# Kernel tuning notes

Hardware: AMD Instinct MI355X
Metric: run time of the kernel (lower is better)

The kernel has to match this reference:

```python
import jax, jax.numpy as jnp
from jax import lax
import numpy as np

N, C, H, W = 8, 128, 96, 96
G, K = 8, 3                      # groups, kernel_size
GC = C // G                      # group channels = 16
STRIDE, PAD, DIL = 1, 1, 1
OFFSET_SCALE = 1.0
OM_DIM = int(np.ceil(G * K * K * 3 / 8) * 8)   # 216 (== G*K*K*3, no padding)
GN_EPS = 1e-5


def setup_inputs() -> dict:
    key = jax.random.key(0)
    ks = jax.random.split(key, 7)
    inp = {
        "input": jax.random.normal(ks[0], (N, C, H, W), dtype=jnp.float32),
        # depthwise conv (Conv2d groups=C): OIHW with I=1
        "dw_w": jax.random.normal(ks[1], (C, 1, K, K), dtype=jnp.float32) * 0.1,
        "dw_b": jax.random.normal(ks[2], (C,), dtype=jnp.float32) * 0.05,
        # GroupNorm(num_groups=1) affine params
        "gn_w": jnp.ones((C,), dtype=jnp.float32),
        "gn_b": jnp.zeros((C,), dtype=jnp.float32),
        # offset_mask Linear (module zero-inits; use small random for a meaningful test)
        "om_w": jax.random.normal(ks[3], (OM_DIM, C), dtype=jnp.float32) * 0.02,
        "om_b": jax.random.normal(ks[4], (OM_DIM,), dtype=jnp.float32) * 0.02,
    }
    return inp


def _dcnv4_forward(x, dw_w, dw_b, gn_w, gn_b, om_w, om_b):
    # x: (N, C, H, W)
    # ---- offset/mask branch: depthwise conv -> GroupNorm(1) -> GELU -> Linear
    x1 = lax.conv_general_dilated(
        x, dw_w, window_strides=(1, 1), padding=[(1, 1), (1, 1)],
        feature_group_count=C, dimension_numbers=("NCHW", "OIHW", "NCHW"))
    x1 = x1 + dw_b[None, :, None, None]
    mu = jnp.mean(x1, axis=(1, 2, 3), keepdims=True)
    var = jnp.var(x1, axis=(1, 2, 3), keepdims=True)
    x1 = (x1 - mu) * lax.rsqrt(var + GN_EPS)
    x1 = x1 * gn_w[None, :, None, None] + gn_b[None, :, None, None]
    x1 = jax.nn.gelu(x1, approximate=False)
    x1 = jnp.transpose(x1, (0, 2, 3, 1))                     # (N,H,W,C)
    om = jnp.einsum("nhwc,oc->nhwo", x1, om_w) + om_b        # (N,H,W,216)

    K2 = K * K
    om = om[..., : G * K2 * 3].reshape(N, H, W, G, K2 * 3)
    offs = om[..., : 2 * K2].reshape(N, H, W, G, K2, 2)      # (dx, dy) per point
    mask = om[..., 2 * K2:]                                  # (N,H,W,G,K2), no softmax in DCNv4

    # ---- sampling locations (pixel coords in the unpadded input, zeros outside)
    ky, kx = jnp.meshgrid(jnp.arange(K), jnp.arange(K), indexing="ij")
    base_y = ((ky - (K - 1) / 2.0) * DIL).reshape(-1).astype(jnp.float32)  # (K2,)
    base_x = ((kx - (K - 1) / 2.0) * DIL).reshape(-1).astype(jnp.float32)
    ctr_y = jnp.arange(H, dtype=jnp.float32) * STRIDE - PAD + DIL * (K - 1) / 2.0
    ctr_x = jnp.arange(W, dtype=jnp.float32) * STRIDE - PAD + DIL * (K - 1) / 2.0
    loc_y = ctr_y[None, :, None, None, None] + (base_y + offs[..., 1]) * OFFSET_SCALE
    loc_x = ctr_x[None, None, :, None, None] + (base_x + offs[..., 0]) * OFFSET_SCALE

    # ---- grouped bilinear gather
    xv = jnp.transpose(x, (0, 2, 3, 1)).reshape(N, H, W, G, GC)   # values, channels-last
    y0 = jnp.floor(loc_y)
    x0 = jnp.floor(loc_x)
    ly = loc_y - y0
    lx = loc_x - x0
    y0i = y0.astype(jnp.int32)
    x0i = x0.astype(jnp.int32)
    n_idx = jnp.arange(N)[:, None, None, None, None]
    g_idx = jnp.arange(G)[None, None, None, :, None]

    def gather(yi, xi):
        valid = (yi >= 0) & (yi < H) & (xi >= 0) & (xi < W)
        yc = jnp.clip(yi, 0, H - 1)
        xc = jnp.clip(xi, 0, W - 1)
        v = xv[n_idx, yc, xc, g_idx]                 # (N,H,W,G,K2,GC)
        return v * valid[..., None].astype(xv.dtype)

    samp = (gather(y0i,     x0i)     * ((1 - ly) * (1 - lx))[..., None]
          + gather(y0i,     x0i + 1) * ((1 - ly) * lx)[..., None]
          + gather(y0i + 1, x0i)     * (ly * (1 - lx))[..., None]
          + gather(y0i + 1, x0i + 1) * (ly * lx)[..., None])

    out = jnp.sum(samp * mask[..., None], axis=4)    # (N,H,W,G,GC)
    out = out.reshape(N, H, W, C)
    return jnp.transpose(out, (0, 3, 1, 2))          # (N,C,H,W)


def reference(input, dw_w, dw_b, gn_w, gn_b, om_w, om_b):
    return _dcnv4_forward(input, dw_w, dw_b, gn_w, gn_b, om_w, om_b)
```

## Files before the change

kernel.cpp:

```cpp
#include <hip/hip_runtime.h>

#define N_   8
#define C_   128
#define H_   96
#define W_   96
#define G_   8
#define GC_  16
#define HW_  (H_ * W_)
#define CHW_ (C_ * HW_)
#define OM_  216
#define OMP_ 224
#define OMROWS2_ 112
#define EPS_ 1e-5f
#define BLKS_PER_N_ 1152

typedef short bf16x8 __attribute__((ext_vector_type(8)));
typedef float f32x4 __attribute__((ext_vector_type(4)));

static __device__ __forceinline__ unsigned short f2bf(float f) {
  unsigned int u = __float_as_uint(f);
  unsigned int r = (u + 0x7fffu + ((u >> 16) & 1u)) >> 16;
  return (unsigned short)r;
}
static __device__ __forceinline__ float lo_bf(unsigned int u) {
  return __uint_as_float(u << 16);
}
static __device__ __forceinline__ float hi_bf(unsigned int u) {
  return __uint_as_float(u & 0xffff0000u);
}

__global__ __launch_bounds__(256) void k_front(const float* __restrict__ x,
                                               const float* __restrict__ dw_w,
                                               const float* __restrict__ dw_b,
                                               float* __restrict__ xg,
                                               unsigned short* __restrict__ x1b,
                                               float2* __restrict__ partials) {
  __shared__ float tile_c[32][33];
  __shared__ float tile_a[32][33];
  __shared__ float ls[4], lq[4];
  int tx = threadIdx.x;
  int ty = threadIdx.y;
  int p0 = blockIdx.x * 32;
  int c0 = blockIdx.y * 32;
  int n = blockIdx.z;
  int p = p0 + tx;
  int h = p / W_;
  int w = p - h * W_;

  float s = 0.0f, q = 0.0f;
#pragma unroll
  for (int i = 0; i < 4; ++i) {
    int c = c0 + ty + i * 8;
    const float* wp = dw_w + c * 9;
    const float* xp = x + (n * C_ + c) * HW_;
    float acc = dw_b[c];
    float center = 0.0f;
#pragma unroll
    for (int dy = 0; dy < 3; ++dy) {
#pragma unroll
      for (int dx = 0; dx < 3; ++dx) {
        int yy = h + dy - 1;
        int xx = w + dx - 1;
        bool v = (yy >= 0) & (yy < H_) & (xx >= 0) & (xx < W_);
        float xin = v ? xp[yy * W_ + xx] : 0.0f;
        if (dy == 1 && dx == 1) center = xin;
        acc = fmaf(xin, wp[dy * 3 + dx], acc);
      }
    }
    tile_c[ty + i * 8][tx] = center;
    tile_a[ty + i * 8][tx] = acc;
    s += acc;
    q += acc * acc;
  }

  int tid = ty * 32 + tx;
#pragma unroll
  for (int o = 32; o > 0; o >>= 1) {
    s += __shfl_down(s, o);
    q += __shfl_down(q, o);
  }
  int lane = tid & 63;
  int wv = tid >> 6;
  if (lane == 0) { ls[wv] = s; lq[wv] = q; }
  __syncthreads();
  if (tid == 0) {
    int bid = blockIdx.x + 288 * blockIdx.y + BLKS_PER_N_ * n;
    partials[bid] = make_float2(ls[0] + ls[1] + ls[2] + ls[3],
                                lq[0] + lq[1] + lq[2] + lq[3]);
  }

  int c = c0 + tx;
  int g = c >> 4;
  int cc = c & 15;
#pragma unroll
  for (int i = 0; i < 4; ++i) {
    int pp = p0 + ty + i * 8;
    xg[(((size_t)(n * G_ + g) * HW_) + pp) * GC_ + cc] = tile_c[tx][ty + i * 8];
    x1b[((size_t)(n * HW_) + pp) * C_ + c] = f2bf(tile_a[tx][ty + i * 8]);
  }
}

__global__ __launch_bounds__(256) void k_stats(const float2* __restrict__ partials,
                                               float* __restrict__ stats) {
  int n = blockIdx.x;
  int tid = threadIdx.x;
  const float2* p = partials + n * BLKS_PER_N_;
  float s = 0.0f, q = 0.0f;
  for (int i = tid; i < BLKS_PER_N_; i += 256) {
    float2 v = p[i];
    s += v.x;
    q += v.y;
  }
#pragma unroll
  for (int o = 32; o > 0; o >>= 1) {
    s += __shfl_down(s, o);
    q += __shfl_down(q, o);
  }
  __shared__ float ls[4], lq[4];
  int lane = tid & 63;
  int wv = tid >> 6;
  if (lane == 0) { ls[wv] = s; lq[wv] = q; }
  __syncthreads();
  if (tid == 0) {
    stats[n * 2 + 0] = ls[0] + ls[1] + ls[2] + ls[3];
    stats[n * 2 + 1] = lq[0] + lq[1] + lq[2] + lq[3];
  }
}

__global__ __launch_bounds__(256) void k_prep(const float* __restrict__ om_w,
                                              const float* __restrict__ om_b,
                                              unsigned short* __restrict__ A,
                                              float* __restrict__ biasp) {
  int idx = blockIdx.x * 256 + threadIdx.x;
  int o = idx >> 7;
  int cix = idx & 127;
  int g = o / 28;
  int k = o - g * 28;
  float v = (k < 27) ? om_w[(g * 27 + k) * C_ + cix] : 0.0f;
  A[idx] = f2bf(v);
  if (cix == 0) biasp[o] = (k < 27) ? om_b[g * 27 + k] : 0.0f;
}

__global__ __launch_bounds__(256) void k_gemm_mfma(const unsigned short* __restrict__ Bt,
                                                   const unsigned short* __restrict__ A,
                                                   const float* __restrict__ biasp,
                                                   const float* __restrict__ stats,
                                                   const float* __restrict__ gn_w,
                                                   const float* __restrict__ gn_b,
                                                   unsigned int* __restrict__ om2) {
  __shared__ unsigned short Bl[128 * 136];
  int tid = threadIdx.x;
  int pb = blockIdx.x;
  int n = blockIdx.y;
  int p0 = pb * 128;

  float sum = stats[n * 2 + 0];
  float ssq = stats[n * 2 + 1];
  const float inv = 1.0f / (float)CHW_;
  float mean = sum * inv;
  float var = ssq * inv - mean * mean;
  float rstd = rsqrtf(var + EPS_);
  int cbase = (tid & 15) * 8;
  float a8[8], b8[8];
#pragma unroll
  for (int j = 0; j < 8; ++j) {
    float gw = gn_w[cbase + j];
    float gb = gn_b[cbase + j];
    a8[j] = rstd * gw;
    b8[j] = gb - mean * rstd * gw;
  }

  const unsigned short* src = Bt + ((size_t)n * HW_ + p0) * C_;
#pragma unroll
  for (int i = 0; i < 8; ++i) {
    int idx = i * 256 + tid;
    int row = idx >> 4;
    int col = idx & 15;
    uint4 raw = *(const uint4*)(src + row * C_ + col * 8);
    unsigned int d[4] = {raw.x, raw.y, raw.z, raw.w};
    unsigned int od[4];
#pragma unroll
    for (int t = 0; t < 4; ++t) {
      float v0 = lo_bf(d[t]);
      float v1 = hi_bf(d[t]);
      float z0 = fmaf(v0, a8[2 * t], b8[2 * t]);
      float z1 = fmaf(v1, a8[2 * t + 1], b8[2 * t + 1]);
      float g0 = 0.5f * z0 * (1.0f + erff(z0 * 0.70710678118654752f));
      float g1 = 0.5f * z1 * (1.0f + erff(z1 * 0.70710678118654752f));
      od[t] = (unsigned int)f2bf(g0) | ((unsigned int)f2bf(g1) << 16);
    }
    uint4 packed = {od[0], od[1], od[2], od[3]};
    *(uint4*)(&Bl[row * 136 + col * 8]) = packed;
  }
  __syncthreads();

  int wave = tid >> 6;
  int lane = tid & 63;
  int quad = lane >> 4;
  int l16 = lane & 15;
  int pw = wave * 32;

  bf16x8 bfrag[2][4];
#pragma unroll
  for (int st = 0; st < 2; ++st) {
    int prow = pw + st * 16 + l16;
#pragma unroll
    for (int kk = 0; kk < 4; ++kk)
      bfrag[st][kk] = *(const bf16x8*)(&Bl[prow * 136 + kk * 32 + quad * 8]);
  }

  for (int ot = 0; ot < 14; ++ot) {
    const unsigned short* Ap = A + (ot * 16 + l16) * C_ + quad * 8;
    bf16x8 afrag[4];
#pragma unroll
    for (int kk = 0; kk < 4; ++kk)
      afrag[kk] = *(const bf16x8*)(Ap + kk * 32);

    f32x4 acc[2] = {{0.f, 0.f, 0.f, 0.f}, {0.f, 0.f, 0.f, 0.f}};
#pragma unroll
    for (int st = 0; st < 2; ++st)
#pragma unroll
      for (int kk = 0; kk < 4; ++kk)
        acc[st] = __builtin_amdgcn_mfma_f32_16x16x32_bf16(afrag[kk], bfrag[st][kk], acc[st], 0, 0, 0);

    int o0 = ot * 16 + quad * 4;
    float4 bv = *(const float4*)(biasp + o0);
#pragma unroll
    for (int st = 0; st < 2; ++st) {
      int p = p0 + pw + st * 16 + l16;
      unsigned int pk0 = (unsigned int)f2bf(acc[st][0] + bv.x) |
                         ((unsigned int)f2bf(acc[st][1] + bv.y) << 16);
      unsigned int pk1 = (unsigned int)f2bf(acc[st][2] + bv.z) |
                         ((unsigned int)f2bf(acc[st][3] + bv.w) << 16);
      unsigned int* Cp = om2 + ((size_t)n * OMROWS2_ + (o0 >> 1)) * HW_ + p;
      Cp[0] = pk0;
      Cp[HW_] = pk1;
    }
  }
}

__global__ __launch_bounds__(256) void k_sample(const float* __restrict__ xg,
                                                const unsigned int* __restrict__ om2,
                                                float* __restrict__ out) {
  __shared__ float4 s_w[9 * 64];
  __shared__ int4   s_a[9 * 64];

  int tid = threadIdx.x;
  int ord = blockIdx.x;
  int n = ord & 7;
  int t2 = ord >> 3;
  int g = t2 & 7;
  int pb = t2 >> 3;
  int p0 = pb * 64;

  const unsigned int* omb = om2 + ((size_t)n * OMROWS2_ + g * 14) * HW_ + p0;
  for (int j = tid; j < 576; j += 256) {
    int pt = j >> 6;
    int px = j & 63;
    int p = p0 + px;
    int h = p / W_;
    int w = p - h * W_;
    unsigned int od = omb[pt * HW_ + px];
    float offx = lo_bf(od);
    float offy = hi_bf(od);
    unsigned int md = omb[(9 + (pt >> 1)) * HW_ + px];
    float m = (pt & 1) ? hi_bf(md) : lo_bf(md);
    float locy = (float)(h + pt / 3 - 1) + offy;
    float locx = (float)(w + pt % 3 - 1) + offx;
    float y0f = floorf(locy);
    float x0f = floorf(locx);
    float ly = locy - y0f;
    float lx = locx - x0f;
    int y0 = (int)y0f;
    int x0 = (int)x0f;
    int y1 = y0 + 1;
    int x1 = x0 + 1;
    bool vy0 = (y0 >= 0) & (y0 < H_);
    bool vy1 = (y1 >= 0) & (y1 < H_);
    bool vx0 = (x0 >= 0) & (x0 < W_);
    bool vx1 = (x1 >= 0) & (x1 < W_);
    int yc0 = min(max(y0, 0), H_ - 1);
    int yc1 = min(max(y1, 0), H_ - 1);
    int xc0 = min(max(x0, 0), W_ - 1);
    int xc1 = min(max(x1, 0), W_ - 1);
    float t0 = (1.0f - ly) * m;
    float t1 = ly * m;
    float u0 = 1.0f - lx;
    float4 wv;
    wv.x = (vy0 & vx0) ? t0 * u0 : 0.0f;
    wv.y = (vy0 & vx1) ? t0 * lx : 0.0f;
    wv.z = (vy1 & vx0) ? t1 * u0 : 0.0f;
    wv.w = (vy1 & vx1) ? t1 * lx : 0.0f;
    int4 av;
    av.x = (yc0 * W_ + xc0) * GC_;
    av.y = (yc0 * W_ + xc1) * GC_;
    av.z = (yc1 * W_ + xc0) * GC_;
    av.w = (yc1 * W_ + xc1) * GC_;
    s_w[j] = wv;
    s_a[j] = av;
  }
  __syncthreads();

  int px_l = tid >> 2;
  int ch = tid & 3;
  int p = p0 + px_l;
  const float* xb = xg + ((size_t)(n * G_ + g) * HW_) * GC_ + ch * 4;

  float4 acc = {0.0f, 0.0f, 0.0f, 0.0f};
#pragma unroll
  for (int pt = 0; pt < 9; ++pt) {
    float4 wv = s_w[pt * 64 + px_l];
    int4 av = s_a[pt * 64 + px_l];
    float4 s00 = *(const float4*)(xb + av.x);
    float4 s01 = *(const float4*)(xb + av.y);
    float4 s10 = *(const float4*)(xb + av.z);
    float4 s11 = *(const float4*)(xb + av.w);
    acc.x = fmaf(wv.x, s00.x, acc.x); acc.y = fmaf(wv.x, s00.y, acc.y);
    acc.z = fmaf(wv.x, s00.z, acc.z); acc.w = fmaf(wv.x, s00.w, acc.w);
    acc.x = fmaf(wv.y, s01.x, acc.x); acc.y = fmaf(wv.y, s01.y, acc.y);
    acc.z = fmaf(wv.y, s01.z, acc.z); acc.w = fmaf(wv.y, s01.w, acc.w);
    acc.x = fmaf(wv.z, s10.x, acc.x); acc.y = fmaf(wv.z, s10.y, acc.y);
    acc.z = fmaf(wv.z, s10.z, acc.z); acc.w = fmaf(wv.z, s10.w, acc.w);
    acc.x = fmaf(wv.w, s11.x, acc.x); acc.y = fmaf(wv.w, s11.y, acc.y);
    acc.z = fmaf(wv.w, s11.z, acc.z); acc.w = fmaf(wv.w, s11.w, acc.w);
  }

  float* op = out + ((size_t)(n * C_ + g * GC_ + ch * 4)) * HW_ + p;
  op[0 * HW_] = acc.x;
  op[1 * HW_] = acc.y;
  op[2 * HW_] = acc.z;
  op[3 * HW_] = acc.w;
}

extern "C" void kernel_launch(void* const* d_in, const int* in_sizes, int n_in,
                              void* d_out, int out_size, void* d_ws, size_t ws_size,
                              hipStream_t stream) {
  const float* x    = (const float*)d_in[0];
  const float* dw_w = (const float*)d_in[1];
  const float* dw_b = (const float*)d_in[2];
  const float* gn_w = (const float*)d_in[3];
  const float* gn_b = (const float*)d_in[4];
  const float* om_w = (const float*)d_in[5];
  const float* om_b = (const float*)d_in[6];
  float* out = (float*)d_out;

  float* xg = (float*)d_ws;
  unsigned short* x1b = (unsigned short*)(xg + (size_t)N_ * CHW_);
  unsigned int* om2 = (unsigned int*)(x1b + (size_t)N_ * CHW_);
  float* stats = (float*)(om2 + (size_t)N_ * OMROWS2_ * HW_);
  float2* partials = (float2*)(stats + 16);
  unsigned short* Abf = (unsigned short*)(partials + N_ * BLKS_PER_N_);
  float* biasp = (float*)(Abf + OMP_ * C_);

  k_front<<<dim3(HW_ / 32, C_ / 32, N_), dim3(32, 8), 0, stream>>>(
      x, dw_w, dw_b, xg, x1b, partials);
  k_stats<<<N_, 256, 0, stream>>>(partials, stats);
  k_prep<<<(OMP_ * C_) / 256, 256, 0, stream>>>(om_w, om_b, Abf, biasp);
  k_gemm_mfma<<<dim3(HW_ / 128, N_), 256, 0, stream>>>(
      x1b, Abf, biasp, stats, gn_w, gn_b, om2);
  k_sample<<<9216, 256, 0, stream>>>(xg, om2, out);
}
```

Measured before the change: 210.3 us.

## Store sampling values in bf16 and fetch horizontal pixel pairs per row

The channels-last grouped copy of the input used for bilinear sampling is now written as bf16 instead of fp32, halving its write and gather traffic. The sampler now issues one 16-byte load per row that covers two adjacent pixels' worth of channels. The two column weights are remapped onto a clamped base column, and partial sums are combined with a lane shuffle. This cuts the number of gather instructions and the shared-memory address storage, at the cost of bf16 rounding of the sampled values and some extra shuffles.

```diff
diff --git a/kernel.cpp b/kernel.cpp
--- a/kernel.cpp
+++ b/kernel.cpp
@@ -32,7 +32,7 @@
 __global__ __launch_bounds__(256) void k_front(const float* __restrict__ x,
                                                const float* __restrict__ dw_w,
                                                const float* __restrict__ dw_b,
-                                               float* __restrict__ xg,
+                                               unsigned short* __restrict__ xgb,
                                                unsigned short* __restrict__ x1b,
                                                float2* __restrict__ partials) {
   __shared__ float tile_c[32][33];
@@ -95,7 +95,7 @@
 #pragma unroll
   for (int i = 0; i < 4; ++i) {
     int pp = p0 + ty + i * 8;
-    xg[(((size_t)(n * G_ + g) * HW_) + pp) * GC_ + cc] = tile_c[tx][ty + i * 8];
+    xgb[(((size_t)(n * G_ + g) * HW_) + pp) * GC_ + cc] = f2bf(tile_c[tx][ty + i * 8]);
     x1b[((size_t)(n * HW_) + pp) * C_ + c] = f2bf(tile_a[tx][ty + i * 8]);
   }
 }
@@ -239,11 +239,11 @@
   }
 }
 
-__global__ __launch_bounds__(256) void k_sample(const float* __restrict__ xg,
+__global__ __launch_bounds__(256) void k_sample(const unsigned short* __restrict__ xgb,
                                                 const unsigned int* __restrict__ om2,
                                                 float* __restrict__ out) {
   __shared__ float4 s_w[9 * 64];
-  __shared__ int4   s_a[9 * 64];
+  __shared__ int2   s_a[9 * 64];
 
   int tid = threadIdx.x;
   int ord = blockIdx.x;
@@ -279,57 +279,68 @@
     bool vy1 = (y1 >= 0) & (y1 < H_);
     bool vx0 = (x0 >= 0) & (x0 < W_);
     bool vx1 = (x1 >= 0) & (x1 < W_);
-    int yc0 = min(max(y0, 0), H_ - 1);
-    int yc1 = min(max(y1, 0), H_ - 1);
-    int xc0 = min(max(x0, 0), W_ - 1);
-    int xc1 = min(max(x1, 0), W_ - 1);
     float t0 = (1.0f - ly) * m;
     float t1 = ly * m;
     float u0 = 1.0f - lx;
+    float w00 = (vy0 & vx0) ? t0 * u0 : 0.0f;
+    float w01 = (vy0 & vx1) ? t0 * lx : 0.0f;
+    float w10 = (vy1 & vx0) ? t1 * u0 : 0.0f;
+    float w11 = (vy1 & vx1) ? t1 * lx : 0.0f;
+    int yc0 = min(max(y0, 0), H_ - 1);
+    int yc1 = min(max(y1, 0), H_ - 1);
+    int xs  = min(max(x0, 0), W_ - 2);
+    int idx0 = min(max(x0, 0), W_ - 1) - xs;
+    int idx1 = min(max(x1, 0), W_ - 1) - xs;
     float4 wv;
-    wv.x = (vy0 & vx0) ? t0 * u0 : 0.0f;
-    wv.y = (vy0 & vx1) ? t0 * lx : 0.0f;
-    wv.z = (vy1 & vx0) ? t1 * u0 : 0.0f;
-    wv.w = (vy1 & vx1) ? t1 * lx : 0.0f;
-    int4 av;
-    av.x = (yc0 * W_ + xc0) * GC_;
-    av.y = (yc0 * W_ + xc1) * GC_;
-    av.z = (yc1 * W_ + xc0) * GC_;
-    av.w = (yc1 * W_ + xc1) * GC_;
+    wv.x = (idx0 == 0 ? w00 : 0.0f) + (idx1 == 0 ? w01 : 0.0f);
+    wv.y = (idx0 == 1 ? w00 : 0.0f) + (idx1 == 1 ? w01 : 0.0f);
+    wv.z = (idx0 == 0 ? w10 : 0.0f) + (idx1 == 0 ? w11 : 0.0f);
+    wv.w = (idx0 == 1 ? w10 : 0.0f) + (idx1 == 1 ? w11 : 0.0f);
+    int2 av;
+    av.x = (yc0 * W_ + xs) * GC_;
+    av.y = (yc1 * W_ + xs) * GC_;
     s_w[j] = wv;
     s_a[j] = av;
   }
   __syncthreads();
 
   int px_l = tid >> 2;
-  int ch = tid & 3;
+  int sub = tid & 3;
+  int rowhalf = sub >> 1;
+  int chunk = sub & 1;
   int p = p0 + px_l;
-  const float* xb = xg + ((size_t)(n * G_ + g) * HW_) * GC_ + ch * 4;
-
-  float4 acc = {0.0f, 0.0f, 0.0f, 0.0f};
+  const unsigned short* xbb = xgb + ((size_t)(n * G_ + g) * HW_) * GC_;
+
+  float acc[8] = {0, 0, 0, 0, 0, 0, 0, 0};
 #pragma unroll
   for (int pt = 0; pt < 9; ++pt) {
     float4 wv = s_w[pt * 64 + px_l];
-    int4 av = s_a[pt * 64 + px_l];
-    float4 s00 = *(const float4*)(xb + av.x);
-    float4 s01 = *(const float4*)(xb + av.y);
-    float4 s10 = *(const float4*)(xb + av.z);
-    float4 s11 = *(const float4*)(xb + av.w);
-    acc.x = fmaf(wv.x, s00.x, acc.x); acc.y = fmaf(wv.x, s00.y, acc.y);
-    acc.z = fmaf(wv.x, s00.z, acc.z); acc.w = fmaf(wv.x, s00.w, acc.w);
-    acc.x = fmaf(wv.y, s01.x, acc.x); acc.y = fmaf(wv.y, s01.y, acc.y);
-    acc.z = fmaf(wv.y, s01.z, acc.z); acc.w = fmaf(wv.y, s01.w, acc.w);
-    acc.x = fmaf(wv.z, s10.x, acc.x); acc.y = fmaf(wv.z, s10.y, acc.y);
-    acc.z = fmaf(wv.z, s10.z, acc.z); acc.w = fmaf(wv.z, s10.w, acc.w);
-    acc.x = fmaf(wv.w, s11.x, acc.x); acc.y = fmaf(wv.w, s11.y, acc.y);
-    acc.z = fmaf(wv.w, s11.z, acc.z); acc.w = fmaf(wv.w, s11.w, acc.w);
-  }
-
-  float* op = out + ((size_t)(n * C_ + g * GC_ + ch * 4)) * HW_ + p;
-  op[0 * HW_] = acc.x;
-  op[1 * HW_] = acc.y;
-  op[2 * HW_] = acc.z;
-  op[3 * HW_] = acc.w;
+    int2 av = s_a[pt * 64 + px_l];
+    float w0 = rowhalf ? wv.y : wv.x;
+    float w1 = rowhalf ? wv.w : wv.z;
+    uint4 r0 = *(const uint4*)(xbb + av.x + sub * 8);
+    uint4 r1 = *(const uint4*)(xbb + av.y + sub * 8);
+    unsigned int d0[4] = {r0.x, r0.y, r0.z, r0.w};
+    unsigned int d1[4] = {r1.x, r1.y, r1.z, r1.w};
+#pragma unroll
+    for (int t = 0; t < 4; ++t) {
+      acc[2 * t]     = fmaf(w0, lo_bf(d0[t]), acc[2 * t]);
+      acc[2 * t + 1] = fmaf(w0, hi_bf(d0[t]), acc[2 * t + 1]);
+    }
+#pragma unroll
+    for (int t = 0; t < 4; ++t) {
+      acc[2 * t]     = fmaf(w1, lo_bf(d1[t]), acc[2 * t]);
+      acc[2 * t + 1] = fmaf(w1, hi_bf(d1[t]), acc[2 * t + 1]);
+    }
+  }
+
+#pragma unroll
+  for (int i = 0; i < 8; ++i) acc[i] += __shfl_xor(acc[i], 2);
+
+  int ch = chunk * 8 + rowhalf * 4;
+  float* op = out + ((size_t)(n * C_ + g * GC_ + ch)) * HW_ + p;
+#pragma unroll
+  for (int r = 0; r < 4; ++r) op[r * HW_] = acc[rowhalf * 4 + r];
 }
 
 extern "C" void kernel_launch(void* const* d_in, const int* in_sizes, int n_in,
@@ -344,8 +355,8 @@
   const float* om_b = (const float*)d_in[6];
   float* out = (float*)d_out;
 
-  float* xg = (float*)d_ws;
-  unsigned short* x1b = (unsigned short*)(xg + (size_t)N_ * CHW_);
+  unsigned short* xgb = (unsigned short*)d_ws;
+  unsigned short* x1b = xgb + (size_t)N_ * CHW_;
   unsigned int* om2 = (unsigned int*)(x1b + (size_t)N_ * CHW_);
   float* stats = (float*)(om2 + (size_t)N_ * OMROWS2_ * HW_);
   float2* partials = (float2*)(stats + 16);
@@ -353,10 +364,10 @@
   float* biasp = (float*)(Abf + OMP_ * C_);
 
   k_front<<<dim3(HW_ / 32, C_ / 32, N_), dim3(32, 8), 0, stream>>>(
-      x, dw_w, dw_b, xg, x1b, partials);
+      x, dw_w, dw_b, xgb, x1b, partials);
   k_stats<<<N_, 256, 0, stream>>>(partials, stats);
   k_prep<<<(OMP_ * C_) / 256, 256, 0, stream>>>(om_w, om_b, Abf, biasp);
   k_gemm_mfma<<<dim3(HW_ / 128, N_), 256, 0, stream>>>(
       x1b, Abf, biasp, stats, gn_w, gn_b, om2);
-  k_sample<<<9216, 256, 0, stream>>>(xg, om2, out);
-}
+  k_sample<<<9216, 256, 0, stream>>>(xgb, om2, out);
+}
```

Result: faster. 204.6 us (-2.7%).
